# Optimization experiments

Measured on AMD Instinct MI355X. Metric: run time of the kernel, lower is better.

Reference implementation:

```python
import jax, jax.numpy as jnp
import numpy as np

EPS = 1e-12  # F.normalize clamp


def _agnn_prop(x, src, dst, beta, num_nodes):
    """AGNNConv propagation: beta*cos-sim edge logits, softmax per target node, scatter-sum."""
    norm = jnp.linalg.norm(x, axis=-1, keepdims=True)
    xn = x / jnp.maximum(norm, EPS)                       # [N, H] unit rows
    logits = beta * jnp.sum(xn[src] * xn[dst], axis=-1)   # [E] cosine similarity * beta
    m = jax.ops.segment_max(logits, dst, num_segments=num_nodes)
    e = jnp.exp(logits - m[dst])
    s = jax.ops.segment_sum(e, dst, num_segments=num_nodes)
    alpha = e / s[dst]                                    # segment softmax over incoming edges
    return jax.ops.segment_sum(x[src] * alpha[:, None], dst, num_segments=num_nodes)


def setup_inputs() -> dict:
    key = jax.random.key(0)
    k1, k2, k3 = jax.random.split(key, 3)
    N, F_IN, H, E = 100000, 128, 64, 1600000
    x = jax.random.normal(k1, (N, F_IN), dtype=jnp.float32)
    edge_index = jax.random.randint(k2, (2, E), 0, N, dtype=jnp.int64)
    W1 = jax.random.normal(k3, (F_IN, H), dtype=jnp.float32) * (1.0 / np.sqrt(F_IN))
    b1 = jnp.zeros((H,), dtype=jnp.float32)
    beta2 = jnp.ones((1,), dtype=jnp.float32)  # AGNNConv(requires_grad=True) beta, init 1.0
    return {"x": x, "edge_index": edge_index, "W1": W1, "b1": b1, "beta2": beta2}


def reference(x, edge_index, W1, b1, beta2):
    N = x.shape[0]
    # AGNNConv adds self loops by default
    loops = jnp.arange(N, dtype=edge_index.dtype)
    src = jnp.concatenate([edge_index[0], loops])
    dst = jnp.concatenate([edge_index[1], loops])
    # dropout is identity in eval mode; self.layers is empty so only lin1 + two props run
    h = x @ W1 + b1                                  # [N, H]
    h = _agnn_prop(h, src, dst, jnp.float32(1.0), N)  # prop1: beta fixed at 1
    h = _agnn_prop(h, src, dst, beta2[0], N)          # prop2: learnable beta
    return jax.nn.log_softmax(h, axis=1)
```

## Files before the change

### kernel.cpp

```cpp
#include <hip/hip_runtime.h>
#include <math.h>

#define FIN 128
#define HDIM 64

#define EB 8192
#define B2SHIFT 9
#define B2 (1 << B2SHIFT)
#define SRCBITS 17
#define SRCMASK ((1u << SRCBITS) - 1u)

typedef __attribute__((ext_vector_type(8))) short short8_t;
typedef __attribute__((ext_vector_type(4))) float f32x4;
typedef _Float16 h2_t __attribute__((ext_vector_type(2)));

__device__ __forceinline__ float2 h2f2(unsigned u) {
    h2_t h = __builtin_bit_cast(h2_t, u);
    return make_float2((float)h.x, (float)h.y);
}
__device__ __forceinline__ unsigned f2h2(float a, float b) {
    h2_t h; h.x = (_Float16)a; h.y = (_Float16)b;
    return __builtin_bit_cast(unsigned, h);
}
__device__ __forceinline__ unsigned short f2h1(float a) {
    _Float16 h = (_Float16)a;
    return __builtin_bit_cast(unsigned short, h);
}

__device__ __forceinline__ void split_bf16(float f, unsigned short& hi, unsigned short& lo) {
    unsigned b = __builtin_bit_cast(unsigned, f);
    hi = (unsigned short)(b >> 16);
    float fh = __builtin_bit_cast(float, b & 0xFFFF0000u);
    float fl = f - fh;
    lo = (unsigned short)(__builtin_bit_cast(unsigned, fl) >> 16);
}

__device__ __forceinline__ float dot8(uint4 v, const float* hd) {
    float2 a = h2f2(v.x), b = h2f2(v.y), c = h2f2(v.z), d = h2f2(v.w);
    float p = a.x * hd[0];
    p = fmaf(a.y, hd[1], p);
    p = fmaf(b.x, hd[2], p);
    p = fmaf(b.y, hd[3], p);
    p = fmaf(c.x, hd[4], p);
    p = fmaf(c.y, hd[5], p);
    p = fmaf(d.x, hd[6], p);
    p = fmaf(d.y, hd[7], p);
    return p;
}
__device__ __forceinline__ void acc8(float w, uint4 v, float* a) {
    float2 f0 = h2f2(v.x), f1 = h2f2(v.y), f2 = h2f2(v.z), f3 = h2f2(v.w);
    a[0] = fmaf(w, f0.x, a[0]); a[1] = fmaf(w, f0.y, a[1]);
    a[2] = fmaf(w, f1.x, a[2]); a[3] = fmaf(w, f1.y, a[3]);
    a[4] = fmaf(w, f2.x, a[4]); a[5] = fmaf(w, f2.y, a[5]);
    a[6] = fmaf(w, f3.x, a[6]); a[7] = fmaf(w, f3.y, a[7]);
}


__global__ __launch_bounds__(256) void p1_hist(
    const int* __restrict__ ei, int* __restrict__ ph,
    int E, int Etot, int NB, int nblk)
{
    __shared__ int h[256];
    h[threadIdx.x] = 0;
    __syncthreads();
    const int base = blockIdx.x * EB;
    const int end = min(base + EB, Etot);
    for (int e = base + (int)threadIdx.x; e < end; e += 256) {
        int d = (e < E) ? ei[E + e] : (e - E);
        atomicAdd(&h[d >> B2SHIFT], 1);
    }
    __syncthreads();
    if ((int)threadIdx.x < NB) ph[threadIdx.x * nblk + blockIdx.x] = h[threadIdx.x];
}

__global__ __launch_bounds__(256) void p1_scanA(
    int* __restrict__ ph, int* __restrict__ btot, int nblk)
{
    __shared__ int wpart[4];
    const int b = blockIdx.x;
    const int t = threadIdx.x, lane = t & 63, w = t >> 6;
    int v = (t < nblk) ? ph[b * nblk + t] : 0;
    int s = v;
#pragma unroll
    for (int off = 1; off < 64; off <<= 1) {
        int u = __shfl_up(s, off, 64);
        if (lane >= off) s += u;
    }
    if (lane == 63) wpart[w] = s;
    __syncthreads();
    int wex = 0;
#pragma unroll
    for (int i = 0; i < 3; ++i) if (i < w) wex += wpart[i];
    if (t < nblk) ph[b * nblk + t] = wex + s - v;
    if (t == 255) btot[b] = wex + s;
}

__global__ __launch_bounds__(256) void p1_scanB(
    const int* __restrict__ btot, int* __restrict__ bbase,
    int* __restrict__ offsets, int NB, int N)
{
    __shared__ int wpart[4];
    const int t = threadIdx.x, lane = t & 63, w = t >> 6;
    int v = (t < NB) ? btot[t] : 0;
    int s = v;
#pragma unroll
    for (int off = 1; off < 64; off <<= 1) {
        int u = __shfl_up(s, off, 64);
        if (lane >= off) s += u;
    }
    if (lane == 63) wpart[w] = s;
    __syncthreads();
    int wex = 0;
#pragma unroll
    for (int i = 0; i < 3; ++i) if (i < w) wex += wpart[i];
    if (t < NB) bbase[t] = wex + s - v;
    if (t == 255) { bbase[NB] = wex + s; offsets[N] = wex + s; }
}

__global__ __launch_bounds__(256) void p2_scatter(
    const int* __restrict__ ei, const int* __restrict__ ph,
    const int* __restrict__ bbase, unsigned* __restrict__ pairs,
    int E, int Etot, int NB, int nblk)
{
    __shared__ int cur[256];
    if ((int)threadIdx.x < NB)
        cur[threadIdx.x] = bbase[threadIdx.x] + ph[threadIdx.x * nblk + blockIdx.x];
    __syncthreads();
    const int base = blockIdx.x * EB;
    const int end = min(base + EB, Etot);
    for (int e = base + (int)threadIdx.x; e < end; e += 256) {
        int s, d;
        if (e < E) { s = ei[e]; d = ei[E + e]; }
        else       { s = e - E; d = s; }
        int pos = atomicAdd(&cur[d >> B2SHIFT], 1);
        pairs[pos] = ((unsigned)(d & (B2 - 1)) << SRCBITS) | (unsigned)s;
    }
}

__global__ __launch_bounds__(256) void p3_csr(
    const unsigned* __restrict__ pairs, const int* __restrict__ bbase,
    int* __restrict__ offsets, int* __restrict__ csr, int N)
{
    __shared__ int hist[B2];
    __shared__ int wp[4];
    const int b = blockIdx.x;
    const int p0 = bbase[b], p1 = bbase[b + 1];
    const int dbase = b << B2SHIFT;
    const int lane = threadIdx.x & 63, w = threadIdx.x >> 6;
    hist[threadIdx.x] = 0; hist[threadIdx.x + 256] = 0;
    __syncthreads();
    for (int i = p0 + (int)threadIdx.x; i < p1; i += 256)
        atomicAdd(&hist[pairs[i] >> SRCBITS], 1);
    __syncthreads();
    const int v0 = hist[2 * threadIdx.x], v1 = hist[2 * threadIdx.x + 1];
    const int t = v0 + v1;
    int s = t;
#pragma unroll
    for (int off = 1; off < 64; off <<= 1) {
        int u = __shfl_up(s, off, 64);
        if (lane >= off) s += u;
    }
    if (lane == 63) wp[w] = s;
    __syncthreads();
    int wex = 0;
#pragma unroll
    for (int i = 0; i < 3; ++i) if (i < w) wex += wp[i];
    const int tex = wex + (s - t);
    const int e0 = tex, e1 = tex + v0;
    const int d0 = dbase + 2 * (int)threadIdx.x, d1 = d0 + 1;
    if (d0 < N) offsets[d0] = p0 + e0;
    if (d1 < N) offsets[d1] = p0 + e1;
    __syncthreads();
    hist[2 * threadIdx.x] = e0; hist[2 * threadIdx.x + 1] = e1;
    __syncthreads();
    for (int i = p0 + (int)threadIdx.x; i < p1; i += 256) {
        unsigned pk = pairs[i];
        int pos = p0 + atomicAdd(&hist[pk >> SRCBITS], 1);
        csr[pos] = (int)(pk & SRCMASK);
    }
}

__global__ __launch_bounds__(256) void gemm_mfma_k(
    const float* __restrict__ x, const float* __restrict__ W,
    const float* __restrict__ b, unsigned short* __restrict__ hn,
    float* __restrict__ nrm, int n)
{
    __shared__ uint4 sB[2][4][4][64];
    for (int idx = threadIdx.x; idx < 2048; idx += 256) {
        int lanei = idx & 63;
        int f = idx >> 6;
        int nt = f & 3, kc = (f >> 2) & 3, hl = f >> 4;
        int col = nt * 16 + (lanei & 15);
        int kb  = kc * 32 + (lanei >> 4) * 8;
        unsigned u[4];
#pragma unroll
        for (int jj = 0; jj < 4; ++jj) {
            unsigned short h0, l0, h1, l1;
            split_bf16(W[(size_t)(kb + 2 * jj)     * HDIM + col], h0, l0);
            split_bf16(W[(size_t)(kb + 2 * jj + 1) * HDIM + col], h1, l1);
            u[jj] = hl ? ((unsigned)l0 | ((unsigned)l1 << 16))
                       : ((unsigned)h0 | ((unsigned)h1 << 16));
        }
        uint4 q; q.x = u[0]; q.y = u[1]; q.z = u[2]; q.w = u[3];
        sB[hl][kc][nt][lanei] = q;
    }
    __syncthreads();

    const int lane = threadIdx.x & 63;
    const int l15 = lane & 15, l4 = lane >> 4;
    const int gw = (int)((blockIdx.x * 256 + threadIdx.x) >> 6);
    const int nw = (int)((gridDim.x * 256) >> 6);
    const int ntiles = (n + 15) >> 4;

    const float bc0 = b[l15], bc1 = b[16 + l15], bc2 = b[32 + l15], bc3 = b[48 + l15];

    for (int tile = gw; tile < ntiles; tile += nw) {
        const int rowbase = tile << 4;
        int arow = rowbase + l15; if (arow >= n) arow = n - 1;
        const float* xp = x + (size_t)arow * FIN + l4 * 8;

        f32x4 acc0 = {bc0, bc0, bc0, bc0};
        f32x4 acc1 = {bc1, bc1, bc1, bc1};
        f32x4 acc2 = {bc2, bc2, bc2, bc2};
        f32x4 acc3 = {bc3, bc3, bc3, bc3};

#pragma unroll
        for (int kc = 0; kc < 4; ++kc) {
            float4 xa = *(const float4*)(xp + kc * 32);
            float4 xb = *(const float4*)(xp + kc * 32 + 4);
            float v[8] = {xa.x, xa.y, xa.z, xa.w, xb.x, xb.y, xb.z, xb.w};
            short8_t ah, al;
#pragma unroll
            for (int j = 0; j < 8; ++j) {
                unsigned bb = __builtin_bit_cast(unsigned, v[j]);
                ah[j] = (short)(bb >> 16);
                float fl = v[j] - __builtin_bit_cast(float, bb & 0xFFFF0000u);
                al[j] = (short)(__builtin_bit_cast(unsigned, fl) >> 16);
            }
#pragma unroll
            for (int nt = 0; nt < 4; ++nt) {
                short8_t bh = __builtin_bit_cast(short8_t, sB[0][kc][nt][lane]);
                short8_t bl = __builtin_bit_cast(short8_t, sB[1][kc][nt][lane]);
                f32x4* pacc = (nt == 0) ? &acc0 : (nt == 1) ? &acc1 : (nt == 2) ? &acc2 : &acc3;
                *pacc = __builtin_amdgcn_mfma_f32_16x16x32_bf16(ah, bh, *pacc, 0, 0, 0);
                *pacc = __builtin_amdgcn_mfma_f32_16x16x32_bf16(al, bh, *pacc, 0, 0, 0);
                *pacc = __builtin_amdgcn_mfma_f32_16x16x32_bf16(ah, bl, *pacc, 0, 0, 0);
            }
        }

        float ss0 = acc0.x*acc0.x + acc1.x*acc1.x + acc2.x*acc2.x + acc3.x*acc3.x;
        float ss1 = acc0.y*acc0.y + acc1.y*acc1.y + acc2.y*acc2.y + acc3.y*acc3.y;
        float ss2 = acc0.z*acc0.z + acc1.z*acc1.z + acc2.z*acc2.z + acc3.z*acc3.z;
        float ss3 = acc0.w*acc0.w + acc1.w*acc1.w + acc2.w*acc2.w + acc3.w*acc3.w;
#pragma unroll
        for (int m = 1; m < 16; m <<= 1) {
            ss0 += __shfl_xor(ss0, m, 64);
            ss1 += __shfl_xor(ss1, m, 64);
            ss2 += __shfl_xor(ss2, m, 64);
            ss3 += __shfl_xor(ss3, m, 64);
        }
        float n0 = sqrtf(ss0), n1 = sqrtf(ss1), n2 = sqrtf(ss2), n3 = sqrtf(ss3);
        float r0 = 1.0f / fmaxf(n0, 1e-12f), r1 = 1.0f / fmaxf(n1, 1e-12f);
        float r2 = 1.0f / fmaxf(n2, 1e-12f), r3 = 1.0f / fmaxf(n3, 1e-12f);
        const int rowb = rowbase + l4 * 4;
        if (l15 == 0) {
            if (rowb + 0 < n) nrm[rowb + 0] = n0;
            if (rowb + 1 < n) nrm[rowb + 1] = n1;
            if (rowb + 2 < n) nrm[rowb + 2] = n2;
            if (rowb + 3 < n) nrm[rowb + 3] = n3;
        }
#pragma unroll
        for (int nt = 0; nt < 4; ++nt) {
            f32x4 a = (nt == 0) ? acc0 : (nt == 1) ? acc1 : (nt == 2) ? acc2 : acc3;
            const int col = nt * 16 + l15;
            if (rowb + 0 < n) hn[(size_t)(rowb + 0) * HDIM + col] = f2h1(a.x * r0);
            if (rowb + 1 < n) hn[(size_t)(rowb + 1) * HDIM + col] = f2h1(a.y * r1);
            if (rowb + 2 < n) hn[(size_t)(rowb + 2) * HDIM + col] = f2h1(a.z * r2);
            if (rowb + 3 < n) hn[(size_t)(rowb + 3) * HDIM + col] = f2h1(a.w * r3);
        }
    }
}

__global__ __launch_bounds__(256) void prop_k(
    const unsigned short* __restrict__ hn, const float* __restrict__ nrm,
    const int* __restrict__ offsets, const int* __restrict__ csr,
    const float* __restrict__ beta_ptr,
    unsigned short* __restrict__ hn_out, float* __restrict__ nrm_out,
    float* __restrict__ lsm_out, int n)
{
    const int lane = threadIdx.x & 63;
    const int sl = lane & 7;
    const int wid = (int)((blockIdx.x * 256 + threadIdx.x) >> 6);
    int d = wid * 8 + (lane >> 3);
    const bool dvalid = d < n;
    if (!dvalid) d = n - 1;
    const float beta = beta_ptr ? beta_ptr[0] : 1.0f;
    const float shift = fabsf(beta);

    const uint4 hdu = *(const uint4*)(hn + ((size_t)d << 6) + (sl << 3));
    float hd[8];
    { float2 f0 = h2f2(hdu.x), f1 = h2f2(hdu.y), f2 = h2f2(hdu.z), f3 = h2f2(hdu.w);
      hd[0]=f0.x; hd[1]=f0.y; hd[2]=f1.x; hd[3]=f1.y;
      hd[4]=f2.x; hd[5]=f2.y; hd[6]=f3.x; hd[7]=f3.y; }

    const int i0 = offsets[d], i1 = offsets[d + 1];
    float acc[8] = {0,0,0,0,0,0,0,0};
    float ssum = 0.f;

    int e = i0;
    for (; e + 1 < i1; e += 2) {
        const int s0 = csr[e], s1 = csr[e + 1];
        const uint4 va = *(const uint4*)(hn + ((size_t)s0 << 6) + (sl << 3));
        const uint4 vb = *(const uint4*)(hn + ((size_t)s1 << 6) + (sl << 3));
        const float na = nrm[s0], nb = nrm[s1];
        float p0 = dot8(va, hd);
        float p1 = dot8(vb, hd);
        p0 += __shfl_xor(p0, 1, 64); p1 += __shfl_xor(p1, 1, 64);
        p0 += __shfl_xor(p0, 2, 64); p1 += __shfl_xor(p1, 2, 64);
        p0 += __shfl_xor(p0, 4, 64); p1 += __shfl_xor(p1, 4, 64);
        const float ev0 = __expf(beta * p0 - shift);
        const float ev1 = __expf(beta * p1 - shift);
        acc8(ev0 * na, va, acc);
        acc8(ev1 * nb, vb, acc);
        ssum += ev0 + ev1;
    }
    if (e < i1) {
        const int s0 = csr[e];
        const uint4 va = *(const uint4*)(hn + ((size_t)s0 << 6) + (sl << 3));
        const float na = nrm[s0];
        float p0 = dot8(va, hd);
        p0 += __shfl_xor(p0, 1, 64);
        p0 += __shfl_xor(p0, 2, 64);
        p0 += __shfl_xor(p0, 4, 64);
        const float ev0 = __expf(beta * p0 - shift);
        acc8(ev0 * na, va, acc);
        ssum += ev0;
    }

    const float rs = 1.0f / ssum;
    float o[8];
#pragma unroll
    for (int j = 0; j < 8; ++j) o[j] = acc[j] * rs;

    if (lsm_out) {
        float mx = o[0];
#pragma unroll
        for (int j = 1; j < 8; ++j) mx = fmaxf(mx, o[j]);
        mx = fmaxf(mx, __shfl_xor(mx, 1, 64));
        mx = fmaxf(mx, __shfl_xor(mx, 2, 64));
        mx = fmaxf(mx, __shfl_xor(mx, 4, 64));
        float es = 0.f;
#pragma unroll
        for (int j = 0; j < 8; ++j) es += __expf(o[j] - mx);
        es += __shfl_xor(es, 1, 64);
        es += __shfl_xor(es, 2, 64);
        es += __shfl_xor(es, 4, 64);
        const float ls = mx + __logf(es);
        if (dvalid) {
            float* op = lsm_out + ((size_t)d << 6) + (sl << 3);
            *(float4*)(op)     = make_float4(o[0]-ls, o[1]-ls, o[2]-ls, o[3]-ls);
            *(float4*)(op + 4) = make_float4(o[4]-ls, o[5]-ls, o[6]-ls, o[7]-ls);
        }
    } else {
        float ss = 0.f;
#pragma unroll
        for (int j = 0; j < 8; ++j) ss = fmaf(o[j], o[j], ss);
        ss += __shfl_xor(ss, 1, 64);
        ss += __shfl_xor(ss, 2, 64);
        ss += __shfl_xor(ss, 4, 64);
        const float norm = sqrtf(ss);
        const float rinv = 1.0f / fmaxf(norm, 1e-12f);
        if (dvalid) {
            uint4 q;
            q.x = f2h2(o[0] * rinv, o[1] * rinv);
            q.y = f2h2(o[2] * rinv, o[3] * rinv);
            q.z = f2h2(o[4] * rinv, o[5] * rinv);
            q.w = f2h2(o[6] * rinv, o[7] * rinv);
            *(uint4*)(hn_out + ((size_t)d << 6) + (sl << 3)) = q;
            if (sl == 0) nrm_out[d] = norm;
        }
    }
}

extern "C" void kernel_launch(void* const* d_in, const int* in_sizes, int n_in,
                              void* d_out, int out_size, void* d_ws, size_t ws_size,
                              hipStream_t stream)
{
    const float* x     = (const float*)d_in[0];
    const int*   ei    = (const int*)d_in[1];
    const float* W1    = (const float*)d_in[2];
    const float* b1    = (const float*)d_in[3];
    const float* beta2 = (const float*)d_in[4];
    float* out = (float*)d_out;

    const int N    = in_sizes[0] / FIN;
    const int E    = in_sizes[1] / 2;
    const int Etot = E + N;
    const int NB   = (N + B2 - 1) >> B2SHIFT;
    const int nblk = (Etot + EB - 1) / EB;

    unsigned short* hn1h = (unsigned short*)d_ws;
    unsigned short* hn2h = hn1h + (size_t)N * HDIM;
    float* nrm1    = (float*)(hn2h + (size_t)N * HDIM);
    float* nrm2    = nrm1 + N;
    int*   offsets = (int*)(nrm2 + N);
    int*   csr     = offsets + (N + 1);
    int*   ph      = csr + Etot;
    int*   bbase   = ph + 256 * nblk;
    int*   btot    = bbase + 257;
    unsigned* pairs = (unsigned*)hn2h;

    const dim3 blk(256);

    p1_hist<<<nblk, blk, 0, stream>>>(ei, ph, E, Etot, NB, nblk);
    p1_scanA<<<NB, blk, 0, stream>>>(ph, btot, nblk);
    p1_scanB<<<1, blk, 0, stream>>>(btot, bbase, offsets, NB, N);
    p2_scatter<<<nblk, blk, 0, stream>>>(ei, ph, bbase, pairs, E, Etot, NB, nblk);
    p3_csr<<<NB, blk, 0, stream>>>(pairs, bbase, offsets, csr, N);

    const int ntiles = (N + 15) >> 4;
    gemm_mfma_k<<<(ntiles + 3) / 4, blk, 0, stream>>>(x, W1, b1, hn1h, nrm1, N);

    const int pblocks = (N + 31) / 32;
    prop_k<<<pblocks, blk, 0, stream>>>(hn1h, nrm1, offsets, csr, nullptr,
                                        hn2h, nrm2, nullptr, N);
    prop_k<<<pblocks, blk, 0, stream>>>(hn2h, nrm2, offsets, csr, beta2,
                                        nullptr, nullptr, out, N);
}
```

Before: 249.3 us.

## Sort destination nodes by degree to balance edge work within wavefronts

Builds a degree histogram during CSR construction, scans it, and creates a permutation of nodes grouped by in-degree. Both propagation kernels then map lanes to nodes through this permutation so that nodes sharing a wavefront have similar edge counts, reducing divergence in the edge loop. This adds two small kernels, a memset, contended global atomics on few bins, and makes per-node loads and output writes non-sequential.

```diff
diff --git a/kernel.cpp b/kernel.cpp
--- a/kernel.cpp
+++ b/kernel.cpp
@@ -9,6 +9,7 @@
 #define B2 (1 << B2SHIFT)
 #define SRCBITS 17
 #define SRCMASK ((1u << SRCBITS) - 1u)
+#define DBINS 256
 
 typedef __attribute__((ext_vector_type(8))) short short8_t;
 typedef __attribute__((ext_vector_type(4))) float f32x4;
@@ -139,7 +140,8 @@
 
 __global__ __launch_bounds__(256) void p3_csr(
     const unsigned* __restrict__ pairs, const int* __restrict__ bbase,
-    int* __restrict__ offsets, int* __restrict__ csr, int N)
+    int* __restrict__ offsets, int* __restrict__ csr,
+    int* __restrict__ dhist, int N)
 {
     __shared__ int hist[B2];
     __shared__ int wp[4];
@@ -168,8 +170,8 @@
     const int tex = wex + (s - t);
     const int e0 = tex, e1 = tex + v0;
     const int d0 = dbase + 2 * (int)threadIdx.x, d1 = d0 + 1;
-    if (d0 < N) offsets[d0] = p0 + e0;
-    if (d1 < N) offsets[d1] = p0 + e1;
+    if (d0 < N) { offsets[d0] = p0 + e0; atomicAdd(&dhist[min(v0, DBINS - 1)], 1); }
+    if (d1 < N) { offsets[d1] = p0 + e1; atomicAdd(&dhist[min(v1, DBINS - 1)], 1); }
     __syncthreads();
     hist[2 * threadIdx.x] = e0; hist[2 * threadIdx.x + 1] = e1;
     __syncthreads();
@@ -177,6 +179,38 @@
         unsigned pk = pairs[i];
         int pos = p0 + atomicAdd(&hist[pk >> SRCBITS], 1);
         csr[pos] = (int)(pk & SRCMASK);
+    }
+}
+
+__global__ __launch_bounds__(256) void p4_scan(
+    const int* __restrict__ dhist, int* __restrict__ dcur)
+{
+    __shared__ int wpart[4];
+    const int t = threadIdx.x, lane = t & 63, w = t >> 6;
+    int v = dhist[t];
+    int s = v;
+#pragma unroll
+    for (int off = 1; off < 64; off <<= 1) {
+        int u = __shfl_up(s, off, 64);
+        if (lane >= off) s += u;
+    }
+    if (lane == 63) wpart[w] = s;
+    __syncthreads();
+    int wex = 0;
+#pragma unroll
+    for (int i = 0; i < 3; ++i) if (i < w) wex += wpart[i];
+    dcur[t] = wex + s - v;
+}
+
+__global__ __launch_bounds__(256) void p5_perm(
+    const int* __restrict__ offsets, int* __restrict__ dcur,
+    int* __restrict__ perm, int N)
+{
+    const int d = blockIdx.x * 256 + threadIdx.x;
+    if (d < N) {
+        const int deg = offsets[d + 1] - offsets[d];
+        const int pos = atomicAdd(&dcur[min(deg, DBINS - 1)], 1);
+        perm[pos] = d;
     }
 }
 
@@ -284,16 +318,16 @@
 __global__ __launch_bounds__(256) void prop_k(
     const unsigned short* __restrict__ hn, const float* __restrict__ nrm,
     const int* __restrict__ offsets, const int* __restrict__ csr,
-    const float* __restrict__ beta_ptr,
+    const int* __restrict__ perm, const float* __restrict__ beta_ptr,
     unsigned short* __restrict__ hn_out, float* __restrict__ nrm_out,
     float* __restrict__ lsm_out, int n)
 {
     const int lane = threadIdx.x & 63;
     const int sl = lane & 7;
     const int wid = (int)((blockIdx.x * 256 + threadIdx.x) >> 6);
-    int d = wid * 8 + (lane >> 3);
-    const bool dvalid = d < n;
-    if (!dvalid) d = n - 1;
+    const int slot = wid * 8 + (lane >> 3);
+    const bool dvalid = slot < n;
+    const int d = perm[dvalid ? slot : (n - 1)];
     const float beta = beta_ptr ? beta_ptr[0] : 1.0f;
     const float shift = fabsf(beta);
 
@@ -408,22 +442,29 @@
     int*   ph      = csr + Etot;
     int*   bbase   = ph + 256 * nblk;
     int*   btot    = bbase + 257;
+    int*   dhist   = btot + 256;
+    int*   dcur    = dhist + DBINS;
+    int*   perm    = dcur + DBINS;
     unsigned* pairs = (unsigned*)hn2h;
 
     const dim3 blk(256);
 
+    hipMemsetAsync(dhist, 0, DBINS * sizeof(int), stream);
     p1_hist<<<nblk, blk, 0, stream>>>(ei, ph, E, Etot, NB, nblk);
     p1_scanA<<<NB, blk, 0, stream>>>(ph, btot, nblk);
     p1_scanB<<<1, blk, 0, stream>>>(btot, bbase, offsets, NB, N);
     p2_scatter<<<nblk, blk, 0, stream>>>(ei, ph, bbase, pairs, E, Etot, NB, nblk);
-    p3_csr<<<NB, blk, 0, stream>>>(pairs, bbase, offsets, csr, N);
+    p3_csr<<<NB, blk, 0, stream>>>(pairs, bbase, offsets, csr, dhist, N);
+
+    p4_scan<<<1, blk, 0, stream>>>(dhist, dcur);
+    p5_perm<<<(N + 255) / 256, blk, 0, stream>>>(offsets, dcur, perm, N);
 
     const int ntiles = (N + 15) >> 4;
     gemm_mfma_k<<<(ntiles + 3) / 4, blk, 0, stream>>>(x, W1, b1, hn1h, nrm1, N);
 
     const int pblocks = (N + 31) / 32;
-    prop_k<<<pblocks, blk, 0, stream>>>(hn1h, nrm1, offsets, csr, nullptr,
+    prop_k<<<pblocks, blk, 0, stream>>>(hn1h, nrm1, offsets, csr, perm, nullptr,
                                         hn2h, nrm2, nullptr, N);
-    prop_k<<<pblocks, blk, 0, stream>>>(hn2h, nrm2, offsets, csr, beta2,
+    prop_k<<<pblocks, blk, 0, stream>>>(hn2h, nrm2, offsets, csr, perm, beta2,
                                         nullptr, nullptr, out, N);
 }
```

Result: slower. 837.0 us (+235.7%).

## Fuse CSR histogram and scatter with fixed-capacity buckets; unroll prop loop by four

Applied to the files above, without the earlier changes.

Replaces the histogram, two-level scan and scatter kernels with one kernel. Each block reserves space in fixed-capacity per-bucket regions (CAP slots) through global atomics, then scatters locally. A single small scan produces the compacted bucket bases. This cuts kernel launches and a full extra pass over the edge list. The risk is overflow if any bucket receives more than CAP edges, and the pairs buffer must now be large enough for NB*CAP entries. The prop loop is also unrolled from two to four edges per iteration to keep more gathers in flight.

```diff
diff --git a/kernel.cpp b/kernel.cpp
--- a/kernel.cpp
+++ b/kernel.cpp
@@ -9,6 +9,7 @@
 #define B2 (1 << B2SHIFT)
 #define SRCBITS 17
 #define SRCMASK ((1u << SRCBITS) - 1u)
+#define CAP 12288
 
 typedef __attribute__((ext_vector_type(8))) short short8_t;
 typedef __attribute__((ext_vector_type(4))) float f32x4;
@@ -56,9 +57,9 @@
 }
 
 
-__global__ __launch_bounds__(256) void p1_hist(
-    const int* __restrict__ ei, int* __restrict__ ph,
-    int E, int Etot, int NB, int nblk)
+__global__ __launch_bounds__(256) void pc_scatter(
+    const int* __restrict__ ei, int* __restrict__ bcur,
+    unsigned* __restrict__ pairs, int E, int Etot, int NB)
 {
     __shared__ int h[256];
     h[threadIdx.x] = 0;
@@ -70,86 +71,59 @@
         atomicAdd(&h[d >> B2SHIFT], 1);
     }
     __syncthreads();
-    if ((int)threadIdx.x < NB) ph[threadIdx.x * nblk + blockIdx.x] = h[threadIdx.x];
-}
-
-__global__ __launch_bounds__(256) void p1_scanA(
-    int* __restrict__ ph, int* __restrict__ btot, int nblk)
-{
-    __shared__ int wpart[4];
-    const int b = blockIdx.x;
-    const int t = threadIdx.x, lane = t & 63, w = t >> 6;
-    int v = (t < nblk) ? ph[b * nblk + t] : 0;
-    int s = v;
-#pragma unroll
-    for (int off = 1; off < 64; off <<= 1) {
-        int u = __shfl_up(s, off, 64);
-        if (lane >= off) s += u;
-    }
-    if (lane == 63) wpart[w] = s;
-    __syncthreads();
-    int wex = 0;
-#pragma unroll
-    for (int i = 0; i < 3; ++i) if (i < w) wex += wpart[i];
-    if (t < nblk) ph[b * nblk + t] = wex + s - v;
-    if (t == 255) btot[b] = wex + s;
-}
-
-__global__ __launch_bounds__(256) void p1_scanB(
-    const int* __restrict__ btot, int* __restrict__ bbase,
-    int* __restrict__ offsets, int NB, int N)
-{
-    __shared__ int wpart[4];
-    const int t = threadIdx.x, lane = t & 63, w = t >> 6;
-    int v = (t < NB) ? btot[t] : 0;
-    int s = v;
-#pragma unroll
-    for (int off = 1; off < 64; off <<= 1) {
-        int u = __shfl_up(s, off, 64);
-        if (lane >= off) s += u;
-    }
-    if (lane == 63) wpart[w] = s;
-    __syncthreads();
-    int wex = 0;
-#pragma unroll
-    for (int i = 0; i < 3; ++i) if (i < w) wex += wpart[i];
-    if (t < NB) bbase[t] = wex + s - v;
-    if (t == 255) { bbase[NB] = wex + s; offsets[N] = wex + s; }
-}
-
-__global__ __launch_bounds__(256) void p2_scatter(
-    const int* __restrict__ ei, const int* __restrict__ ph,
-    const int* __restrict__ bbase, unsigned* __restrict__ pairs,
-    int E, int Etot, int NB, int nblk)
-{
-    __shared__ int cur[256];
-    if ((int)threadIdx.x < NB)
-        cur[threadIdx.x] = bbase[threadIdx.x] + ph[threadIdx.x * nblk + blockIdx.x];
-    __syncthreads();
-    const int base = blockIdx.x * EB;
-    const int end = min(base + EB, Etot);
+    const int cnt = h[threadIdx.x];
+    int rsv = 0;
+    if ((int)threadIdx.x < NB && cnt > 0)
+        rsv = atomicAdd(&bcur[threadIdx.x], cnt);
+    __syncthreads();
+    h[threadIdx.x] = (int)threadIdx.x * CAP + rsv;
+    __syncthreads();
     for (int e = base + (int)threadIdx.x; e < end; e += 256) {
         int s, d;
         if (e < E) { s = ei[e]; d = ei[E + e]; }
         else       { s = e - E; d = s; }
-        int pos = atomicAdd(&cur[d >> B2SHIFT], 1);
+        int pos = atomicAdd(&h[d >> B2SHIFT], 1);
         pairs[pos] = ((unsigned)(d & (B2 - 1)) << SRCBITS) | (unsigned)s;
     }
 }
 
+__global__ __launch_bounds__(256) void pc_scan(
+    const int* __restrict__ bcur, int* __restrict__ bbase,
+    int* __restrict__ offsets, int NB, int N)
+{
+    __shared__ int wpart[4];
+    const int t = threadIdx.x, lane = t & 63, w = t >> 6;
+    int v = (t < NB) ? bcur[t] : 0;
+    int s = v;
+#pragma unroll
+    for (int off = 1; off < 64; off <<= 1) {
+        int u = __shfl_up(s, off, 64);
+        if (lane >= off) s += u;
+    }
+    if (lane == 63) wpart[w] = s;
+    __syncthreads();
+    int wex = 0;
+#pragma unroll
+    for (int i = 0; i < 3; ++i) if (i < w) wex += wpart[i];
+    if (t < NB) bbase[t] = wex + s - v;
+    if (t == NB - 1) { bbase[NB] = wex + s; offsets[N] = wex + s; }
+}
+
 __global__ __launch_bounds__(256) void p3_csr(
-    const unsigned* __restrict__ pairs, const int* __restrict__ bbase,
-    int* __restrict__ offsets, int* __restrict__ csr, int N)
+    const unsigned* __restrict__ pairs, const int* __restrict__ bcur,
+    const int* __restrict__ bbase, int* __restrict__ offsets,
+    int* __restrict__ csr, int N)
 {
     __shared__ int hist[B2];
     __shared__ int wp[4];
     const int b = blockIdx.x;
-    const int p0 = bbase[b], p1 = bbase[b + 1];
+    const int p0in = b * CAP, p1in = p0in + bcur[b];
+    const int p0out = bbase[b];
     const int dbase = b << B2SHIFT;
     const int lane = threadIdx.x & 63, w = threadIdx.x >> 6;
     hist[threadIdx.x] = 0; hist[threadIdx.x + 256] = 0;
     __syncthreads();
-    for (int i = p0 + (int)threadIdx.x; i < p1; i += 256)
+    for (int i = p0in + (int)threadIdx.x; i < p1in; i += 256)
         atomicAdd(&hist[pairs[i] >> SRCBITS], 1);
     __syncthreads();
     const int v0 = hist[2 * threadIdx.x], v1 = hist[2 * threadIdx.x + 1];
@@ -168,14 +142,14 @@
     const int tex = wex + (s - t);
     const int e0 = tex, e1 = tex + v0;
     const int d0 = dbase + 2 * (int)threadIdx.x, d1 = d0 + 1;
-    if (d0 < N) offsets[d0] = p0 + e0;
-    if (d1 < N) offsets[d1] = p0 + e1;
+    if (d0 < N) offsets[d0] = p0out + e0;
+    if (d1 < N) offsets[d1] = p0out + e1;
     __syncthreads();
     hist[2 * threadIdx.x] = e0; hist[2 * threadIdx.x + 1] = e1;
     __syncthreads();
-    for (int i = p0 + (int)threadIdx.x; i < p1; i += 256) {
+    for (int i = p0in + (int)threadIdx.x; i < p1in; i += 256) {
         unsigned pk = pairs[i];
-        int pos = p0 + atomicAdd(&hist[pk >> SRCBITS], 1);
+        int pos = p0out + atomicAdd(&hist[pk >> SRCBITS], 1);
         csr[pos] = (int)(pk & SRCMASK);
     }
 }
@@ -308,30 +282,37 @@
     float ssum = 0.f;
 
     int e = i0;
-    for (; e + 1 < i1; e += 2) {
-        const int s0 = csr[e], s1 = csr[e + 1];
+    for (; e + 3 < i1; e += 4) {
+        const int s0 = csr[e], s1 = csr[e + 1], s2 = csr[e + 2], s3 = csr[e + 3];
         const uint4 va = *(const uint4*)(hn + ((size_t)s0 << 6) + (sl << 3));
         const uint4 vb = *(const uint4*)(hn + ((size_t)s1 << 6) + (sl << 3));
-        const float na = nrm[s0], nb = nrm[s1];
-        float p0 = dot8(va, hd);
-        float p1 = dot8(vb, hd);
-        p0 += __shfl_xor(p0, 1, 64); p1 += __shfl_xor(p1, 1, 64);
-        p0 += __shfl_xor(p0, 2, 64); p1 += __shfl_xor(p1, 2, 64);
-        p0 += __shfl_xor(p0, 4, 64); p1 += __shfl_xor(p1, 4, 64);
+        const uint4 vc = *(const uint4*)(hn + ((size_t)s2 << 6) + (sl << 3));
+        const uint4 vd = *(const uint4*)(hn + ((size_t)s3 << 6) + (sl << 3));
+        const float na = nrm[s0], nb = nrm[s1], nc = nrm[s2], nd = nrm[s3];
+        float p0 = dot8(va, hd), p1 = dot8(vb, hd);
+        float p2 = dot8(vc, hd), p3 = dot8(vd, hd);
+#pragma unroll
+        for (int m = 1; m < 8; m <<= 1) {
+            p0 += __shfl_xor(p0, m, 64); p1 += __shfl_xor(p1, m, 64);
+            p2 += __shfl_xor(p2, m, 64); p3 += __shfl_xor(p3, m, 64);
+        }
         const float ev0 = __expf(beta * p0 - shift);
         const float ev1 = __expf(beta * p1 - shift);
+        const float ev2 = __expf(beta * p2 - shift);
+        const float ev3 = __expf(beta * p3 - shift);
         acc8(ev0 * na, va, acc);
         acc8(ev1 * nb, vb, acc);
-        ssum += ev0 + ev1;
-    }
-    if (e < i1) {
+        acc8(ev2 * nc, vc, acc);
+        acc8(ev3 * nd, vd, acc);
+        ssum += (ev0 + ev1) + (ev2 + ev3);
+    }
+    for (; e < i1; ++e) {
         const int s0 = csr[e];
         const uint4 va = *(const uint4*)(hn + ((size_t)s0 << 6) + (sl << 3));
         const float na = nrm[s0];
         float p0 = dot8(va, hd);
-        p0 += __shfl_xor(p0, 1, 64);
-        p0 += __shfl_xor(p0, 2, 64);
-        p0 += __shfl_xor(p0, 4, 64);
+#pragma unroll
+        for (int m = 1; m < 8; m <<= 1) p0 += __shfl_xor(p0, m, 64);
         const float ev0 = __expf(beta * p0 - shift);
         acc8(ev0 * na, va, acc);
         ssum += ev0;
@@ -405,18 +386,16 @@
     float* nrm2    = nrm1 + N;
     int*   offsets = (int*)(nrm2 + N);
     int*   csr     = offsets + (N + 1);
-    int*   ph      = csr + Etot;
-    int*   bbase   = ph + 256 * nblk;
-    int*   btot    = bbase + 257;
+    int*   bcur    = csr + Etot;
+    int*   bbase   = bcur + 256;
     unsigned* pairs = (unsigned*)hn2h;
 
     const dim3 blk(256);
 
-    p1_hist<<<nblk, blk, 0, stream>>>(ei, ph, E, Etot, NB, nblk);
-    p1_scanA<<<NB, blk, 0, stream>>>(ph, btot, nblk);
-    p1_scanB<<<1, blk, 0, stream>>>(btot, bbase, offsets, NB, N);
-    p2_scatter<<<nblk, blk, 0, stream>>>(ei, ph, bbase, pairs, E, Etot, NB, nblk);
-    p3_csr<<<NB, blk, 0, stream>>>(pairs, bbase, offsets, csr, N);
+    hipMemsetAsync(bcur, 0, 256 * sizeof(int), stream);
+    pc_scatter<<<nblk, blk, 0, stream>>>(ei, bcur, pairs, E, Etot, NB);
+    pc_scan<<<1, blk, 0, stream>>>(bcur, bbase, offsets, NB, N);
+    p3_csr<<<NB, blk, 0, stream>>>(pairs, bcur, bbase, offsets, csr, N);
 
     const int ntiles = (N + 15) >> 4;
     gemm_mfma_k<<<(ntiles + 3) / 4, blk, 0, stream>>>(x, W1, b1, hn1h, nrm1, N);
```

Result: no change. 250.5 us (+0.5%).
